# Performance work log

Hardware: AMD Instinct MI355X
Metric: run time of the kernel (lower is better)

Reference implementation:

```python
import jax, jax.numpy as jnp
import numpy as np
import math

D_MODEL = 1024
N_HEADS = 16
D_KV = 64
INNER = N_HEADS * D_KV
NUM_BUCKETS = 32
MAX_DISTANCE = 128


def _relative_position_bucket(relative_position, bidirectional=True,
                              num_buckets=NUM_BUCKETS, max_distance=MAX_DISTANCE):
    # faithful port of T5Attention._relative_position_bucket
    relative_buckets = jnp.zeros_like(relative_position)
    if bidirectional:
        num_buckets //= 2
        relative_buckets = relative_buckets + (relative_position > 0).astype(jnp.int32) * num_buckets
        relative_position = jnp.abs(relative_position)
    else:
        relative_position = -jnp.minimum(relative_position, jnp.zeros_like(relative_position))
    max_exact = num_buckets // 2
    is_small = relative_position < max_exact
    rp_large = max_exact + (
        jnp.log(relative_position.astype(jnp.float32) / max_exact)
        / math.log(max_distance / max_exact) * (num_buckets - max_exact)
    ).astype(jnp.int32)
    rp_large = jnp.minimum(rp_large, num_buckets - 1)
    return relative_buckets + jnp.where(is_small, relative_position, rp_large)


def compute_bias(rel_bias_table, q_len, k_len):
    # [q_len, k_len] relative positions -> bucket ids -> [1, H, q_len, k_len] bias
    context = jnp.arange(q_len, dtype=jnp.int32)[:, None]
    memory = jnp.arange(k_len, dtype=jnp.int32)[None, :]
    buckets = _relative_position_bucket(memory - context, bidirectional=True)
    values = rel_bias_table[buckets]            # [q, k, H]
    return jnp.transpose(values, (2, 0, 1))[None]  # [1, H, q, k]


def setup_inputs() -> dict:
    key = jax.random.key(0)
    ks = jax.random.split(key, 6)
    B, S = 2, 2048
    scale = 0.02
    return {
        "hidden_states": jax.random.normal(ks[0], (B, S, D_MODEL), jnp.float32),
        # weights stored as [in, out] (torch Linear applies x @ W.T with W [out,in])
        "w_q": jax.random.normal(ks[1], (D_MODEL, INNER), jnp.float32) * scale,
        "w_k": jax.random.normal(ks[2], (D_MODEL, INNER), jnp.float32) * scale,
        "w_v": jax.random.normal(ks[3], (D_MODEL, INNER), jnp.float32) * scale,
        "w_o": jax.random.normal(ks[4], (INNER, D_MODEL), jnp.float32) * scale,
        "rel_bias_table": jax.random.normal(ks[5], (NUM_BUCKETS, N_HEADS), jnp.float32) * scale,
    }


def reference(hidden_states, w_q, w_k, w_v, w_o, rel_bias_table):
    B, S, _ = hidden_states.shape

    def shape(x):  # [B, S, inner] -> [B, H, S, d_kv]
        return jnp.transpose(x.reshape(B, S, N_HEADS, D_KV), (0, 2, 1, 3))

    q = shape(hidden_states @ w_q)  # note: T5 applies no 1/sqrt(d) scaling
    k = shape(hidden_states @ w_k)
    v = shape(hidden_states @ w_v)

    scores = jnp.einsum("bhqd,bhkd->bhqk", q, k)
    position_bias = compute_bias(rel_bias_table, S, S)
    scores = scores + position_bias
    attn = jax.nn.softmax(scores.astype(jnp.float32), axis=-1).astype(scores.dtype)
    ctx = jnp.einsum("bhqk,bhkd->bhqd", attn, v)
    ctx = jnp.transpose(ctx, (0, 2, 1, 3)).reshape(B, S, INNER)
    return ctx @ w_o
```

## Files before the change

### kernel.cpp

```cpp
#include <hip/hip_runtime.h>
#include <math.h>

#define S_LEN 2048
#define DM 1024

typedef __attribute__((ext_vector_type(8))) __bf16 bf16x8;
typedef __attribute__((ext_vector_type(4))) float floatx4;

typedef __attribute__((address_space(1))) const unsigned int g_u32;
typedef __attribute__((address_space(3))) unsigned int l_u32;

__device__ __forceinline__ unsigned short f2bf(float f) {
  union { float f; unsigned int u; } v; v.f = f;
  return (unsigned short)((v.u + 0x7fffu + ((v.u >> 16) & 1u)) >> 16);
}
__device__ __forceinline__ float bf2f(unsigned short u) {
  union { unsigned int u; float f; } v; v.u = ((unsigned int)u) << 16;
  return v.f;
}
__device__ __forceinline__ bf16x8 ld_frag(const unsigned short* p) {
  union { uint4 u; bf16x8 v; } t;
  t.u = *(const uint4*)p;
  return t.v;
}

__global__ void detect_k(const unsigned short* __restrict__ x, int* __restrict__ flag) {
  __shared__ int cnt;
  if (threadIdx.x == 0) cnt = 0;
  __syncthreads();
  int local = 0;
  for (int i = threadIdx.x; i < 4096; i += 256) {
    unsigned short u = x[i];
    int e = (u >> 7) & 0xFF;
    if (e > 140) local++;
  }
  atomicAdd(&cnt, local);
  __syncthreads();
  if (threadIdx.x == 0) *flag = (cnt > 64) ? 1 : 0;
}

__global__ void conv_x(const void* __restrict__ src, unsigned short* __restrict__ dst,
                       const int* __restrict__ flag, int n8) {
  int i = blockIdx.x * 256 + threadIdx.x;
  if (i >= n8) return;
  if (*flag) {
    const float4* s = (const float4*)src;
    float4 a = s[2 * i], b = s[2 * i + 1];
    union { uint4 u4; unsigned short s[8]; } o;
    o.s[0] = f2bf(a.x); o.s[1] = f2bf(a.y); o.s[2] = f2bf(a.z); o.s[3] = f2bf(a.w);
    o.s[4] = f2bf(b.x); o.s[5] = f2bf(b.y); o.s[6] = f2bf(b.z); o.s[7] = f2bf(b.w);
    ((uint4*)dst)[i] = o.u4;
  } else {
    ((uint4*)dst)[i] = ((const uint4*)src)[i];
  }
}

__global__ void transpose_w(const void* __restrict__ s0, const void* __restrict__ s1,
                            const void* __restrict__ s2, const void* __restrict__ s3,
                            unsigned short* __restrict__ Wcat, unsigned short* __restrict__ Wto,
                            const int* __restrict__ flag) {
  __shared__ float tile[32][33];
  const int z = blockIdx.z;
  const void* src = (z == 0) ? s0 : (z == 1) ? s1 : (z == 2) ? s2 : s3;
  unsigned short* dst = (z < 3) ? (Wcat + (size_t)z * 1048576) : Wto;
  const int isf = *flag;
  int x = blockIdx.x * 32 + threadIdx.x;
  int y0 = blockIdx.y * 32;
  for (int i = threadIdx.y; i < 32; i += 8) {
    float v;
    if (isf) v = ((const float*)src)[(size_t)(y0 + i) * DM + x];
    else     v = bf2f(((const unsigned short*)src)[(size_t)(y0 + i) * DM + x]);
    tile[i][threadIdx.x] = v;
  }
  __syncthreads();
  int xo = y0 + threadIdx.x;
  for (int i = threadIdx.y; i < 32; i += 8)
    dst[(size_t)(blockIdx.x * 32 + i) * DM + xo] = f2bf(tile[threadIdx.x][i]);
}

__global__ void bias_k(const void* __restrict__ table, float* __restrict__ out,
                       const int* __restrict__ flag) {
  int idx = blockIdx.x * 256 + threadIdx.x;
  if (idx >= 16 * 4095) return;
  int h = idx / 4095;
  int j = idx - h * 4095;
  int delta = j - 2047;
  int bucket = (delta > 0) ? 16 : 0;
  int ad = (delta < 0) ? -delta : delta;
  int smallv;
  if (ad < 8) smallv = ad;
  else {
    int l = (int)(log((double)ad * 0.125) * (8.0 / log(16.0)));
    smallv = 8 + l;
    if (smallv > 15) smallv = 15;
  }
  bucket += smallv;
  float v;
  if (*flag) v = ((const float*)table)[bucket * 16 + h];
  else       v = bf2f(((const unsigned short*)table)[bucket * 16 + h]);
  out[idx] = v;
}

__global__ __launch_bounds__(256) void gemm_bt(
    const unsigned short* __restrict__ A, const unsigned short* __restrict__ Bt,
    void* __restrict__ C, int mode, const int* __restrict__ flag)
{
  __shared__ __align__(16) unsigned short As[128 * 64];
  __shared__ __align__(16) unsigned short Bs[128 * 64];
  const int tid = threadIdx.x;
  const int lane = tid & 63, wave = tid >> 6;
  const int l16 = lane & 15, quad = lane >> 4;
  const int wm = (wave >> 1) << 6, wn = (wave & 1) << 6;
  const int m0 = blockIdx.y << 7, n0 = blockIdx.x << 7;
  const int lrow = lane >> 3, lcol = (lane & 7) << 3;

  floatx4 acc[4][4] = {};

  for (int k0 = 0; k0 < 1024; k0 += 64) {
    __syncthreads();
#pragma unroll
    for (int i = 0; i < 4; ++i) {
      int r0 = wave * 32 + i * 8;
      __builtin_amdgcn_global_load_lds(
          (g_u32*)(const void*)(A + (size_t)(m0 + r0 + lrow) * 1024 + k0 + lcol),
          (l_u32*)(void*)&As[r0 * 64], 16, 0, 0);
      __builtin_amdgcn_global_load_lds(
          (g_u32*)(const void*)(Bt + (size_t)(n0 + r0 + lrow) * 1024 + k0 + lcol),
          (l_u32*)(void*)&Bs[r0 * 64], 16, 0, 0);
    }
    __syncthreads();
#pragma unroll
    for (int ks = 0; ks < 2; ++ks) {
      bf16x8 a[4], b[4];
#pragma unroll
      for (int mi = 0; mi < 4; ++mi)
        a[mi] = *(const bf16x8*)&As[(wm + mi * 16 + l16) * 64 + ks * 32 + quad * 8];
#pragma unroll
      for (int ni = 0; ni < 4; ++ni)
        b[ni] = *(const bf16x8*)&Bs[(wn + ni * 16 + l16) * 64 + ks * 32 + quad * 8];
#pragma unroll
      for (int mi = 0; mi < 4; ++mi)
#pragma unroll
        for (int ni = 0; ni < 4; ++ni)
          acc[mi][ni] = __builtin_amdgcn_mfma_f32_16x16x32_bf16(a[mi], b[ni], acc[mi][ni], 0, 0, 0);
    }
  }

  if (mode == 0) {
    unsigned short* Cs = (unsigned short*)C;
    const int mat = n0 >> 10;
#pragma unroll
    for (int mi = 0; mi < 4; ++mi)
#pragma unroll
      for (int ni = 0; ni < 4; ++ni)
#pragma unroll
        for (int i = 0; i < 4; ++i) {
          int m = m0 + wm + mi * 16 + quad * 4 + i;
          int n = (n0 & 1023) + wn + ni * 16 + l16;
          int b = m >> 11, s = m & 2047, h = n >> 6, d = n & 63;
          unsigned short v = f2bf(acc[mi][ni][i]);
          if (mat < 2)
            Cs[(size_t)mat * 4194304 + (((size_t)(b * 16 + h)) * 2048 + s) * 64 + d] = v;
          else
            Cs[(size_t)2 * 4194304 + (((size_t)(b * 16 + h)) * 64 + d) * 2048 + s] = v;
        }
  } else {
    const int isf = *flag;
#pragma unroll
    for (int mi = 0; mi < 4; ++mi)
#pragma unroll
      for (int ni = 0; ni < 4; ++ni)
#pragma unroll
        for (int i = 0; i < 4; ++i) {
          int m = m0 + wm + mi * 16 + quad * 4 + i;
          int n = n0 + wn + ni * 16 + l16;
          size_t idx = (size_t)m * 1024 + n;
          float v = acc[mi][ni][i];
          if (isf) ((float*)C)[idx] = v;
          else     ((unsigned short*)C)[idx] = f2bf(v);
        }
  }
}

__global__ __launch_bounds__(256) void gemm_out(
    const unsigned short* __restrict__ A, const unsigned short* __restrict__ Bt,
    void* __restrict__ C, const int* __restrict__ flag)
{
  __shared__ __align__(16) unsigned short As[128 * 64];
  __shared__ __align__(16) unsigned short Bs[64 * 64];
  const int tid = threadIdx.x;
  const int lane = tid & 63, wave = tid >> 6;
  const int l16 = lane & 15, quad = lane >> 4;
  const int wm = (wave >> 1) << 6, wn = (wave & 1) << 5;
  const int m0 = blockIdx.y << 7, n0 = blockIdx.x << 6;
  const int lrow = lane >> 3, lcol = (lane & 7) << 3;

  floatx4 acc[4][2] = {};

  for (int k0 = 0; k0 < 1024; k0 += 64) {
    __syncthreads();
#pragma unroll
    for (int i = 0; i < 4; ++i) {
      int r0 = wave * 32 + i * 8;
      __builtin_amdgcn_global_load_lds(
          (g_u32*)(const void*)(A + (size_t)(m0 + r0 + lrow) * 1024 + k0 + lcol),
          (l_u32*)(void*)&As[r0 * 64], 16, 0, 0);
    }
#pragma unroll
    for (int i = 0; i < 2; ++i) {
      int r0 = wave * 16 + i * 8;
      __builtin_amdgcn_global_load_lds(
          (g_u32*)(const void*)(Bt + (size_t)(n0 + r0 + lrow) * 1024 + k0 + lcol),
          (l_u32*)(void*)&Bs[r0 * 64], 16, 0, 0);
    }
    __syncthreads();
#pragma unroll
    for (int ks = 0; ks < 2; ++ks) {
      bf16x8 a[4], b[2];
#pragma unroll
      for (int mi = 0; mi < 4; ++mi)
        a[mi] = *(const bf16x8*)&As[(wm + mi * 16 + l16) * 64 + ks * 32 + quad * 8];
#pragma unroll
      for (int ni = 0; ni < 2; ++ni)
        b[ni] = *(const bf16x8*)&Bs[(wn + ni * 16 + l16) * 64 + ks * 32 + quad * 8];
#pragma unroll
      for (int mi = 0; mi < 4; ++mi)
#pragma unroll
        for (int ni = 0; ni < 2; ++ni)
          acc[mi][ni] = __builtin_amdgcn_mfma_f32_16x16x32_bf16(a[mi], b[ni], acc[mi][ni], 0, 0, 0);
    }
  }

  const int isf = *flag;
#pragma unroll
  for (int mi = 0; mi < 4; ++mi)
#pragma unroll
    for (int ni = 0; ni < 2; ++ni)
#pragma unroll
      for (int i = 0; i < 4; ++i) {
        int m = m0 + wm + mi * 16 + quad * 4 + i;
        int n = n0 + wn + ni * 16 + l16;
        size_t idx = (size_t)m * 1024 + n;
        float v = acc[mi][ni][i];
        if (isf) ((float*)C)[idx] = v;
        else     ((unsigned short*)C)[idx] = f2bf(v);
      }
}

#define STAGE_KV(kv0)                                                          \
  _Pragma("unroll")                                                           \
  for (int i = 0; i < 4; ++i) {                                               \
    int kr = i * 32 + wave * 8 + (lane >> 3);                                 \
    __builtin_amdgcn_global_load_lds(                                         \
        (g_u32*)(const void*)(Kp + (size_t)((kv0) + kr) * 64 +                \
                              (((lane & 7) ^ (lane >> 3)) << 3)),             \
        (l_u32*)(void*)&Ks[i * 2048 + wave * 512], 16, 0, 0);                 \
    int vd = i * 16 + wave * 4 + (lane >> 4);                                 \
    __builtin_amdgcn_global_load_lds(                                         \
        (g_u32*)(const void*)(Vp + (size_t)vd * S_LEN + (kv0) +               \
                              (((lane & 15) ^ (wave * 4 + (lane >> 4))) << 3)),\
        (l_u32*)(void*)&Vs[i * 2048 + wave * 512], 16, 0, 0);                 \
  }

__global__ __launch_bounds__(256, 2) void attn_k(
    const unsigned short* __restrict__ Q, const unsigned short* __restrict__ K,
    const unsigned short* __restrict__ Vt, const float* __restrict__ bias,
    unsigned short* __restrict__ ctx)
{
  __shared__ __align__(16) unsigned short Ks[128 * 64];
  __shared__ __align__(16) unsigned short Vs[64 * 128];
  __shared__ __align__(16) unsigned short Ps[4][32][136];
  __shared__ float Bls[2176];
  const int tid = threadIdx.x;
  const int lane = tid & 63, wave = tid >> 6;
  const int l16 = lane & 15, quad = lane >> 4;
  const int bh = blockIdx.y;
  const int b = bh >> 4, h = bh & 15;
  const int q0 = blockIdx.x << 7;
  const int wq = wave << 5;

  const unsigned short* Qp = Q + (size_t)bh * S_LEN * 64;
  const unsigned short* Kp = K + (size_t)bh * S_LEN * 64;
  const unsigned short* Vp = Vt + (size_t)bh * 64 * S_LEN;
  const float* biasg = bias + h * 4095 + (1920 - q0);

  STAGE_KV(0);
  for (int i = tid; i < 2175; i += 256)
    Bls[i] = fmaf(biasg[i], 1.44269504f, -24.f);

  bf16x8 qf[2][2];
#pragma unroll
  for (int mi = 0; mi < 2; ++mi)
#pragma unroll
    for (int ks = 0; ks < 2; ++ks)
      qf[mi][ks] = ld_frag(Qp + (size_t)(q0 + wq + mi * 16 + l16) * 64 + ks * 32 + quad * 8);

  float l_run[2][4] = {};
  floatx4 oacc[2][4] = {};

  const int qwb = q0 + wq;
  const int rbase = 127 + l16 - wq - (quad << 2);

  __syncthreads();

  for (int kv0 = 0; kv0 < S_LEN; kv0 += 128) {
    const float Bneg = Bls[0], Bpos = Bls[2174];

    floatx4 sac[2][8] = {};
#pragma unroll
    for (int ks = 0; ks < 2; ++ks) {
      bf16x8 kf[8];
#pragma unroll
      for (int ni = 0; ni < 8; ++ni)
        kf[ni] = *(const bf16x8*)&Ks[(ni * 16 + l16) * 64 +
                                     ((((ks << 2) + quad) ^ (l16 & 7)) << 3)];
#pragma unroll
      for (int mi = 0; mi < 2; ++mi)
#pragma unroll
        for (int ni = 0; ni < 8; ++ni)
          sac[mi][ni] = __builtin_amdgcn_mfma_f32_16x16x32_bf16(qf[mi][ks], kf[ni], sac[mi][ni], 0, 0, 0);
    }

    {
      const int dmin = kv0 - (qwb + 31);
      const int dmax = kv0 + 127 - qwb;
      if (dmin >= 96 || dmax <= -96) {
        const float bc = (dmin >= 96) ? Bpos : Bneg;
#pragma unroll
        for (int mi = 0; mi < 2; ++mi)
#pragma unroll
          for (int i = 0; i < 4; ++i) {
            float sum = 0.f;
#pragma unroll
            for (int ni = 0; ni < 8; ++ni) {
              float e = __builtin_amdgcn_exp2f(fmaf(sac[mi][ni][i], 1.44269504f, bc));
              sac[mi][ni][i] = e; sum += e;
            }
            l_run[mi][i] += sum;
          }
      } else {
#pragma unroll
        for (int mi = 0; mi < 2; ++mi)
#pragma unroll
          for (int i = 0; i < 4; ++i) {
            const int bbase = kv0 + rbase - i - mi * 16;
            float sum = 0.f;
#pragma unroll
            for (int ni = 0; ni < 8; ++ni) {
              float e = __builtin_amdgcn_exp2f(
                  fmaf(sac[mi][ni][i], 1.44269504f, Bls[bbase + ni * 16]));
              sac[mi][ni][i] = e; sum += e;
            }
            l_run[mi][i] += sum;
          }
      }
    }

#pragma unroll
    for (int mi = 0; mi < 2; ++mi)
#pragma unroll
      for (int ni = 0; ni < 8; ++ni)
#pragma unroll
        for (int i = 0; i < 4; ++i)
          Ps[wave][mi * 16 + quad * 4 + i][ni * 16 + l16] = f2bf(sac[mi][ni][i]);

#pragma unroll
    for (int ks2 = 0; ks2 < 4; ++ks2) {
      bf16x8 af[2], vf[4];
#pragma unroll
      for (int mi = 0; mi < 2; ++mi)
        af[mi] = *(const bf16x8*)&Ps[wave][mi * 16 + l16][ks2 * 32 + quad * 8];
#pragma unroll
      for (int ni = 0; ni < 4; ++ni)
        vf[ni] = *(const bf16x8*)&Vs[(ni * 16 + l16) * 128 +
                                     ((((ks2 << 2) + quad) ^ l16) << 3)];
#pragma unroll
      for (int mi = 0; mi < 2; ++mi)
#pragma unroll
        for (int ni = 0; ni < 4; ++ni)
          oacc[mi][ni] = __builtin_amdgcn_mfma_f32_16x16x32_bf16(af[mi], vf[ni], oacc[mi][ni], 0, 0, 0);
    }

    if (kv0 + 128 < S_LEN) {
      __syncthreads();
      STAGE_KV(kv0 + 128);
      __syncthreads();
    }
  }

  float linv[2][4];
#pragma unroll
  for (int mi = 0; mi < 2; ++mi)
#pragma unroll
    for (int i = 0; i < 4; ++i) {
      float ls = l_run[mi][i];
      ls += __shfl_xor(ls, 1);
      ls += __shfl_xor(ls, 2);
      ls += __shfl_xor(ls, 4);
      ls += __shfl_xor(ls, 8);
      linv[mi][i] = 1.f / ls;
    }

#pragma unroll
  for (int mi = 0; mi < 2; ++mi)
#pragma unroll
    for (int ni = 0; ni < 4; ++ni)
#pragma unroll
      for (int i = 0; i < 4; ++i) {
        float v = oacc[mi][ni][i] * linv[mi][i];
        int srow = q0 + wq + mi * 16 + quad * 4 + i;
        ctx[((size_t)(b * 2048 + srow)) * 1024 + h * 64 + ni * 16 + l16] = f2bf(v);
      }
}

extern "C" void kernel_launch(void* const* d_in, const int* in_sizes, int n_in,
                              void* d_out, int out_size, void* d_ws, size_t ws_size,
                              hipStream_t stream) {
  char* ws = (char*)d_ws;
  unsigned short* Xbf  = (unsigned short*)(ws);
  unsigned short* Wcat = (unsigned short*)(ws + 8388608);
  unsigned short* Wto  = (unsigned short*)(ws + 14680064);
  unsigned short* Qb   = (unsigned short*)(ws + 16777216);
  unsigned short* ctx  = (unsigned short*)(ws + 41943040);
  float*          bias = (float*)(ws + 50331648);
  int*            flag = (int*)(ws + 50593792);

  unsigned short* Kb  = Qb + 4194304;
  unsigned short* Vtb = Qb + 8388608;

  detect_k<<<1, 256, 0, stream>>>((const unsigned short*)d_in[0], flag);
  conv_x<<<2048, 256, 0, stream>>>(d_in[0], Xbf, flag, 524288);
  transpose_w<<<dim3(32, 32, 4), dim3(32, 8), 0, stream>>>(
      d_in[1], d_in[2], d_in[3], d_in[4], Wcat, Wto, flag);
  bias_k<<<256, 256, 0, stream>>>(d_in[5], bias, flag);

  gemm_bt<<<dim3(24, 32), 256, 0, stream>>>(Xbf, Wcat, Qb, 0, flag);

  attn_k<<<dim3(16, 32), 256, 0, stream>>>(Qb, Kb, Vtb, bias, ctx);

  gemm_out<<<dim3(16, 32), 256, 0, stream>>>(ctx, Wto, d_out, flag);
}
```

Baseline: 237.5 us.

## Double-buffer K/V tiles in attention and coalesce transposed V stores in QKV GEMM

The attention kernel now uses 64-wide KV tiles held in two LDS buffers, issuing the next tile's async global-to-LDS loads before computing on the current one. This replaces the previous two-barrier load-then-compute step with a single barrier per iteration. The QKV GEMM epilogue for the V matrix now transposes through shared memory and writes 16-byte coalesced rows instead of scattered 2-byte stores. In exchange there are twice as many KV iterations, plus extra barriers and LDS traffic in the GEMM epilogue.

Measured after the change: 230.9 us. -2.8%, faster.

```diff
diff --git a/kernel.cpp b/kernel.cpp
--- a/kernel.cpp
+++ b/kernel.cpp
@@ -105,8 +105,9 @@
     const unsigned short* __restrict__ A, const unsigned short* __restrict__ Bt,
     void* __restrict__ C, int mode, const int* __restrict__ flag)
 {
-  __shared__ __align__(16) unsigned short As[128 * 64];
-  __shared__ __align__(16) unsigned short Bs[128 * 64];
+  __shared__ __align__(16) unsigned short smem[128 * 136];
+  unsigned short* As = smem;
+  unsigned short* Bs = smem + 8192;
   const int tid = threadIdx.x;
   const int lane = tid & 63, wave = tid >> 6;
   const int l16 = lane & 15, quad = lane >> 4;
@@ -149,21 +150,40 @@
   if (mode == 0) {
     unsigned short* Cs = (unsigned short*)C;
     const int mat = n0 >> 10;
-#pragma unroll
-    for (int mi = 0; mi < 4; ++mi)
-#pragma unroll
-      for (int ni = 0; ni < 4; ++ni)
-#pragma unroll
-        for (int i = 0; i < 4; ++i) {
-          int m = m0 + wm + mi * 16 + quad * 4 + i;
-          int n = (n0 & 1023) + wn + ni * 16 + l16;
-          int b = m >> 11, s = m & 2047, h = n >> 6, d = n & 63;
-          unsigned short v = f2bf(acc[mi][ni][i]);
-          if (mat < 2)
-            Cs[(size_t)mat * 4194304 + (((size_t)(b * 16 + h)) * 2048 + s) * 64 + d] = v;
-          else
-            Cs[(size_t)2 * 4194304 + (((size_t)(b * 16 + h)) * 64 + d) * 2048 + s] = v;
+    if (mat < 2) {
+#pragma unroll
+      for (int mi = 0; mi < 4; ++mi)
+#pragma unroll
+        for (int ni = 0; ni < 4; ++ni)
+#pragma unroll
+          for (int i = 0; i < 4; ++i) {
+            int m = m0 + wm + mi * 16 + quad * 4 + i;
+            int n = (n0 & 1023) + wn + ni * 16 + l16;
+            int b = m >> 11, s = m & 2047, h = n >> 6, d = n & 63;
+            Cs[(size_t)mat * 4194304 + (((size_t)(b * 16 + h)) * 2048 + s) * 64 + d] =
+                f2bf(acc[mi][ni][i]);
+          }
+    } else {
+      __syncthreads();
+#pragma unroll
+      for (int mi = 0; mi < 4; ++mi)
+#pragma unroll
+        for (int ni = 0; ni < 4; ++ni) {
+          union { unsigned short s[4]; uint2 u; } w;
+#pragma unroll
+          for (int i = 0; i < 4; ++i) w.s[i] = f2bf(acc[mi][ni][i]);
+          *(uint2*)&smem[(wn + ni * 16 + l16) * 136 + wm + mi * 16 + quad * 4] = w.u;
         }
+      __syncthreads();
+      const int bb = m0 >> 11, s0 = m0 & 2047, nb = n0 & 1023;
+#pragma unroll
+      for (int it = 0; it < 8; ++it) {
+        int r = it * 16 + (tid >> 4);
+        int c = (tid & 15) * 8;
+        uint4 rv = *(const uint4*)&smem[r * 136 + c];
+        *(uint4*)&Cs[(size_t)2 * 4194304 + (size_t)(bb * 1024 + nb + r) * 2048 + s0 + c] = rv;
+      }
+    }
   } else {
     const int isf = *flag;
 #pragma unroll
@@ -247,19 +267,17 @@
       }
 }
 
-#define STAGE_KV(kv0)                                                          \
+#define STAGE_KV(kv0, buf)                                                    \
   _Pragma("unroll")                                                           \
-  for (int i = 0; i < 4; ++i) {                                               \
-    int kr = i * 32 + wave * 8 + (lane >> 3);                                 \
+  for (int i = 0; i < 2; ++i) {                                               \
+    int rr = i * 32 + wave * 8 + (lane >> 3);                                 \
+    int sw = ((lane & 7) ^ (lane >> 3)) << 3;                                 \
     __builtin_amdgcn_global_load_lds(                                         \
-        (g_u32*)(const void*)(Kp + (size_t)((kv0) + kr) * 64 +                \
-                              (((lane & 7) ^ (lane >> 3)) << 3)),             \
-        (l_u32*)(void*)&Ks[i * 2048 + wave * 512], 16, 0, 0);                 \
-    int vd = i * 16 + wave * 4 + (lane >> 4);                                 \
+        (g_u32*)(const void*)(Kp + (size_t)((kv0) + rr) * 64 + sw),           \
+        (l_u32*)(void*)&Ks[buf][i * 2048 + wave * 512], 16, 0, 0);            \
     __builtin_amdgcn_global_load_lds(                                         \
-        (g_u32*)(const void*)(Vp + (size_t)vd * S_LEN + (kv0) +               \
-                              (((lane & 15) ^ (wave * 4 + (lane >> 4))) << 3)),\
-        (l_u32*)(void*)&Vs[i * 2048 + wave * 512], 16, 0, 0);                 \
+        (g_u32*)(const void*)(Vp + (size_t)rr * S_LEN + (kv0) + sw),          \
+        (l_u32*)(void*)&Vs[buf][i * 2048 + wave * 512], 16, 0, 0);            \
   }
 
 __global__ __launch_bounds__(256, 2) void attn_k(
@@ -267,9 +285,9 @@
     const unsigned short* __restrict__ Vt, const float* __restrict__ bias,
     unsigned short* __restrict__ ctx)
 {
-  __shared__ __align__(16) unsigned short Ks[128 * 64];
-  __shared__ __align__(16) unsigned short Vs[64 * 128];
-  __shared__ __align__(16) unsigned short Ps[4][32][136];
+  __shared__ __align__(16) unsigned short Ks[2][4096];
+  __shared__ __align__(16) unsigned short Vs[2][4096];
+  __shared__ __align__(16) unsigned short Ps[4][32][72];
   __shared__ float Bls[2176];
   const int tid = threadIdx.x;
   const int lane = tid & 63, wave = tid >> 6;
@@ -284,7 +302,7 @@
   const unsigned short* Vp = Vt + (size_t)bh * 64 * S_LEN;
   const float* biasg = bias + h * 4095 + (1920 - q0);
 
-  STAGE_KV(0);
+  STAGE_KV(0, 0);
   for (int i = tid; i < 2175; i += 256)
     Bls[i] = fmaf(biasg[i], 1.44269504f, -24.f);
 
@@ -302,28 +320,30 @@
   const int rbase = 127 + l16 - wq - (quad << 2);
 
   __syncthreads();
-
-  for (int kv0 = 0; kv0 < S_LEN; kv0 += 128) {
-    const float Bneg = Bls[0], Bpos = Bls[2174];
-
-    floatx4 sac[2][8] = {};
+  const float Bneg = Bls[0], Bpos = Bls[2174];
+
+  for (int kv0 = 0; kv0 < S_LEN; kv0 += 64) {
+    const int cur = (kv0 >> 6) & 1;
+    if (kv0 + 64 < S_LEN) STAGE_KV(kv0 + 64, cur ^ 1);
+
+    floatx4 sac[2][4] = {};
 #pragma unroll
     for (int ks = 0; ks < 2; ++ks) {
-      bf16x8 kf[8];
-#pragma unroll
-      for (int ni = 0; ni < 8; ++ni)
-        kf[ni] = *(const bf16x8*)&Ks[(ni * 16 + l16) * 64 +
-                                     ((((ks << 2) + quad) ^ (l16 & 7)) << 3)];
+      bf16x8 kf[4];
+#pragma unroll
+      for (int ni = 0; ni < 4; ++ni)
+        kf[ni] = *(const bf16x8*)&Ks[cur][(ni * 16 + l16) * 64 +
+                                          ((((ks << 2) + quad) ^ (l16 & 7)) << 3)];
 #pragma unroll
       for (int mi = 0; mi < 2; ++mi)
 #pragma unroll
-        for (int ni = 0; ni < 8; ++ni)
+        for (int ni = 0; ni < 4; ++ni)
           sac[mi][ni] = __builtin_amdgcn_mfma_f32_16x16x32_bf16(qf[mi][ks], kf[ni], sac[mi][ni], 0, 0, 0);
     }
 
     {
       const int dmin = kv0 - (qwb + 31);
-      const int dmax = kv0 + 127 - qwb;
+      const int dmax = kv0 + 63 - qwb;
       if (dmin >= 96 || dmax <= -96) {
         const float bc = (dmin >= 96) ? Bpos : Bneg;
 #pragma unroll
@@ -332,7 +352,7 @@
           for (int i = 0; i < 4; ++i) {
             float sum = 0.f;
 #pragma unroll
-            for (int ni = 0; ni < 8; ++ni) {
+            for (int ni = 0; ni < 4; ++ni) {
               float e = __builtin_amdgcn_exp2f(fmaf(sac[mi][ni][i], 1.44269504f, bc));
               sac[mi][ni][i] = e; sum += e;
             }
@@ -346,7 +366,7 @@
             const int bbase = kv0 + rbase - i - mi * 16;
             float sum = 0.f;
 #pragma unroll
-            for (int ni = 0; ni < 8; ++ni) {
+            for (int ni = 0; ni < 4; ++ni) {
               float e = __builtin_amdgcn_exp2f(
                   fmaf(sac[mi][ni][i], 1.44269504f, Bls[bbase + ni * 16]));
               sac[mi][ni][i] = e; sum += e;
@@ -359,21 +379,21 @@
 #pragma unroll
     for (int mi = 0; mi < 2; ++mi)
 #pragma unroll
-      for (int ni = 0; ni < 8; ++ni)
+      for (int ni = 0; ni < 4; ++ni)
 #pragma unroll
         for (int i = 0; i < 4; ++i)
           Ps[wave][mi * 16 + quad * 4 + i][ni * 16 + l16] = f2bf(sac[mi][ni][i]);
 
 #pragma unroll
-    for (int ks2 = 0; ks2 < 4; ++ks2) {
+    for (int ks2 = 0; ks2 < 2; ++ks2) {
       bf16x8 af[2], vf[4];
 #pragma unroll
       for (int mi = 0; mi < 2; ++mi)
         af[mi] = *(const bf16x8*)&Ps[wave][mi * 16 + l16][ks2 * 32 + quad * 8];
 #pragma unroll
       for (int ni = 0; ni < 4; ++ni)
-        vf[ni] = *(const bf16x8*)&Vs[(ni * 16 + l16) * 128 +
-                                     ((((ks2 << 2) + quad) ^ l16) << 3)];
+        vf[ni] = *(const bf16x8*)&Vs[cur][(ni * 16 + l16) * 64 +
+                                          ((((ks2 << 2) + quad) ^ (l16 & 7)) << 3)];
 #pragma unroll
       for (int mi = 0; mi < 2; ++mi)
 #pragma unroll
@@ -381,11 +401,7 @@
           oacc[mi][ni] = __builtin_amdgcn_mfma_f32_16x16x32_bf16(af[mi], vf[ni], oacc[mi][ni], 0, 0, 0);
     }
 
-    if (kv0 + 128 < S_LEN) {
-      __syncthreads();
-      STAGE_KV(kv0 + 128);
-      __syncthreads();
-    }
+    __syncthreads();
   }
 
   float linv[2][4];
```
